# Kernel optimization log

Hardware: AMD Instinct MI355X
Metric: run time of the kernel (lower is better)

## Reference

```python
import jax, jax.numpy as jnp
import numpy as np

N_NODES = 100000
IN_F = 128
HID = [128, 128]
EMB = 64
N_EDGES = 3200000


def _glorot(key, fan_in, fan_out):
    lim = np.sqrt(6.0 / (fan_in + fan_out)).astype(np.float32)
    return jax.random.uniform(key, (fan_in, fan_out), jnp.float32, -lim, lim)


def setup_inputs() -> dict:
    key = jax.random.key(0)
    ks = jax.random.split(key, 10)
    h0 = jax.random.normal(ks[0], (N_NODES, IN_F), jnp.float32)
    edge_index = jax.random.randint(ks[1], (2, N_EDGES), 0, N_NODES, jnp.int32)
    edge_weight = jax.random.uniform(ks[2], (N_EDGES,), jnp.float32)
    dims = [(IN_F, HID[0]), (IN_F, HID[0]), (IN_F, HID[0]),
            (HID[0], HID[1]), (HID[0], HID[1]), (HID[1], EMB)]
    out = {"h0": h0, "edge_index": edge_index, "edge_weight": edge_weight}
    for i, (fi, fo) in enumerate(dims):
        out[f"W{i+1}"] = _glorot(ks[3 + i], fi, fo)
        out[f"b{i+1}"] = jnp.zeros((fo,), jnp.float32)
    return out


def gcn_conv(x, W, b, row, col, norm):
    # x: [N,F_in]; row/col/norm already include self-loops and symmetric norm
    h = x @ W                                  # [N, F_out]
    msg = h[row] * norm[:, None]               # gather + scale  [E+N, F_out]
    agg = jax.ops.segment_sum(msg, col, num_segments=x.shape[0])
    return agg + b


def reference(h0, edge_index, edge_weight, W1, b1, W2, b2, W3, b3, W4, b4, W5, b5, W6, b6):
    n = h0.shape[0]
    row, col = edge_index[0], edge_index[1]
    loop = jnp.arange(n, dtype=row.dtype)
    row2 = jnp.concatenate([row, loop])
    col2 = jnp.concatenate([col, loop])
    ew2 = jnp.concatenate([edge_weight, jnp.ones((n,), edge_weight.dtype)])
    # PyG gcn_norm: deg over destination, symmetric D^-1/2 A D^-1/2
    deg = jax.ops.segment_sum(ew2, col2, num_segments=n)
    dis = jnp.where(deg > 0, jax.lax.rsqrt(jnp.maximum(deg, 1e-20)), 0.0)
    norm = dis[row2] * ew2 * dis[col2]

    h1 = jnp.tanh(gcn_conv(h0, W1, b1, row2, col2, norm))
    h2 = jnp.tanh(gcn_conv(h0, W2, b2, row2, col2, norm))
    h3 = jnp.tanh(gcn_conv(h0, W3, b3, row2, col2, norm))
    h123 = h1 * h2 * h3
    h4 = jnp.tanh(gcn_conv(h123, W4, b4, row2, col2, norm))
    h5 = jnp.tanh(gcn_conv(h123, W5, b5, row2, col2, norm))
    h6 = jnp.tanh(gcn_conv(h4 * h5, W6, b6, row2, col2, norm))
    return h6
```

## Files before the change

### kernel.cpp

```cpp
#include <hip/hip_runtime.h>
#include <hip/hip_bf16.h>
#include <hip/hip_fp16.h>

constexpr int FDIM = 128;
#define HSCALE 16384.0f
#define HSCALE_INV (1.0f/16384.0f)
#define ZSCALE 0.125f
#define ZSCALE_COMP (HSCALE_INV * 8.0f)

typedef _Float16 f16x8 __attribute__((ext_vector_type(8)));
typedef float f32x4 __attribute__((ext_vector_type(4)));

constexpr int CHUNK = 4096;
constexpr int B1 = 64;
constexpr int B2 = 64;
constexpr int NC2 = 64;
constexpr int MAXC2 = 20;

__global__ __launch_bounds__(256) void k_p1hist(const int* __restrict__ col,
                                                int* __restrict__ cnt1, int E, int NB1)
{
    __shared__ int h[B1];
    int blk = blockIdx.x, t = threadIdx.x;
    if (t < B1) h[t] = 0;
    __syncthreads();
    int base = blk * CHUNK;
    for (int i = t; i < CHUNK; i += 256) {
        int g = base + i;
        if (g < E) atomicAdd(&h[col[g] >> 11], 1);
    }
    __syncthreads();
    if (t < B1) cnt1[t * NB1 + blk] = h[t];
}

__global__ __launch_bounds__(256) void k_blocksum(const int* __restrict__ cnt,
                                                  int* __restrict__ bsum, int n)
{
    __shared__ int s[256];
    int t = threadIdx.x;
    int i = blockIdx.x * 256 + t;
    s[t] = (i < n) ? cnt[i] : 0;
    __syncthreads();
    for (int o = 128; o > 0; o >>= 1) {
        if (t < o) s[t] += s[t + o];
        __syncthreads();
    }
    if (t == 0) bsum[blockIdx.x] = s[0];
}

__global__ __launch_bounds__(1024) void k_scan_bsum(const int* __restrict__ bsum,
                                                    int* __restrict__ boff, int nb,
                                                    int* __restrict__ out, int n, int total)
{
    __shared__ int s[1024];
    int t = threadIdx.x;
    int v = (t < nb) ? bsum[t] : 0;
    s[t] = v;
    __syncthreads();
    for (int o = 1; o < 1024; o <<= 1) {
        int u = (t >= o) ? s[t - o] : 0;
        __syncthreads();
        s[t] += u;
        __syncthreads();
    }
    if (t < nb) boff[t] = s[t] - v;
    if (t == 0) out[n] = total;
}

__global__ __launch_bounds__(256) void k_offsets(const int* __restrict__ cnt,
                                                 const int* __restrict__ boff,
                                                 int* __restrict__ out, int n)
{
    __shared__ int s[256];
    int t = threadIdx.x;
    int i = blockIdx.x * 256 + t;
    int v = (i < n) ? cnt[i] : 0;
    s[t] = v;
    __syncthreads();
    for (int o = 1; o < 256; o <<= 1) {
        int u = (t >= o) ? s[t - o] : 0;
        __syncthreads();
        s[t] += u;
        __syncthreads();
    }
    if (i < n) out[i] = boff[blockIdx.x] + s[t] - v;
}

__global__ __launch_bounds__(256) void k_p1part(const int* __restrict__ col,
                                                const int* __restrict__ row,
                                                const float* __restrict__ ew,
                                                const int* __restrict__ cnt1,
                                                const int* __restrict__ scan1,
                                                unsigned long long* __restrict__ rec1,
                                                int E, int NB1)
{
    __shared__ unsigned long long stage[CHUNK];
    __shared__ int hcnt[B1], lb[B1], gb[B1], cur[B1];
    int blk = blockIdx.x, t = threadIdx.x;
    if (t < B1) {
        hcnt[t] = cnt1[t * NB1 + blk];
        gb[t]   = scan1[t * NB1 + blk];
    }
    __syncthreads();
    if (t == 0) {
        int run = 0;
        for (int b = 0; b < B1; ++b) { lb[b] = run; run += hcnt[b]; }
    }
    __syncthreads();
    if (t < B1) cur[t] = lb[t];
    __syncthreads();
    int base = blk * CHUNK;
    for (int i = t; i < CHUNK; i += 256) {
        int g = base + i;
        if (g < E) {
            int c = col[g], r = row[g];
            unsigned long long rc = ((unsigned long long)c << 47) |
                                    ((unsigned long long)r << 30) |
                                    (unsigned long long)__half_as_ushort(__float2half(ew[g]));
            int p = atomicAdd(&cur[c >> 11], 1);
            stage[p] = rc;
        }
    }
    __syncthreads();
    int here = min(CHUNK, E - base);
    for (int j = t; j < here; j += 256) {
        unsigned long long rc = stage[j];
        int b = (int)(rc >> 58);
        rec1[gb[b] + (j - lb[b])] = rc;
    }
}

__global__ __launch_bounds__(256) void k_p2hist(const unsigned long long* __restrict__ rec1,
                                                const int* __restrict__ scan1,
                                                int* __restrict__ cnt2, int NB1)
{
    __shared__ int h[B2];
    int b = blockIdx.x / MAXC2, ci = blockIdx.x % MAXC2, t = threadIdx.x;
    int S1 = scan1[b * NB1];
    int S2 = scan1[(b + 1) * NB1];
    int size = S2 - S1;
    for (int c = ci; c * CHUNK < size && c < NC2; c += MAXC2) {
        __syncthreads();
        if (t < B2) h[t] = 0;
        __syncthreads();
        int cb = S1 + c * CHUNK, ce = min(cb + CHUNK, S2);
        for (int i = cb + t; i < ce; i += 256)
            atomicAdd(&h[(int)((rec1[i] >> 52) & 63)], 1);
        __syncthreads();
        if (t < B2) cnt2[(b * B2 + t) * NC2 + c] = h[t];
    }
}

__global__ __launch_bounds__(256) void k_p2part(const unsigned long long* __restrict__ rec1,
                                                const int* __restrict__ scan1,
                                                const int* __restrict__ cnt2,
                                                const int* __restrict__ scan2,
                                                unsigned long long* __restrict__ rec2, int NB1)
{
    __shared__ unsigned long long stage[CHUNK];
    __shared__ int hcnt[B2], lb[B2], gb[B2], cur[B2];
    int b = blockIdx.x / MAXC2, ci = blockIdx.x % MAXC2, t = threadIdx.x;
    int S1 = scan1[b * NB1];
    int S2 = scan1[(b + 1) * NB1];
    int size = S2 - S1;
    for (int c = ci; c * CHUNK < size && c < NC2; c += MAXC2) {
        __syncthreads();
        if (t < B2) {
            hcnt[t] = cnt2[(b * B2 + t) * NC2 + c];
            gb[t]   = scan2[(b * B2 + t) * NC2 + c];
        }
        __syncthreads();
        if (t == 0) {
            int run = 0;
            for (int sb = 0; sb < B2; ++sb) { lb[sb] = run; run += hcnt[sb]; }
        }
        __syncthreads();
        if (t < B2) cur[t] = lb[t];
        __syncthreads();
        int cb = S1 + c * CHUNK, ce = min(cb + CHUNK, S2);
        for (int i = cb + t; i < ce; i += 256) {
            unsigned long long rc = rec1[i];
            int p = atomicAdd(&cur[(int)((rc >> 52) & 63)], 1);
            stage[p] = rc;
        }
        __syncthreads();
        int here = ce - cb;
        for (int j = t; j < here; j += 256) {
            unsigned long long rc = stage[j];
            int sb = (int)((rc >> 52) & 63);
            rec2[gb[sb] + (j - lb[sb])] = rc;
        }
    }
}

__global__ __launch_bounds__(256) void k_p3(const unsigned long long* __restrict__ rec2,
                                            const int* __restrict__ scan2,
                                            int2* __restrict__ ep, int* __restrict__ off,
                                            float* __restrict__ dis, int N, int E)
{
    __shared__ int h[32], lb[32], cur[32];
    __shared__ float dg[32], sdis[32];
    int g = blockIdx.x, t = threadIdx.x;
    int S1 = scan2[g * NC2];
    int S2 = scan2[(g + 1) * NC2];
    if (t < 32) { h[t] = 0; dg[t] = 0.f; }
    __syncthreads();
    for (int i = S1 + t; i < S2; i += 256) {
        unsigned long long rc = rec2[i];
        int nl = (int)((rc >> 47) & 31);
        atomicAdd(&h[nl], 1);
        atomicAdd(&dg[nl], __half2float(__ushort_as_half((unsigned short)(rc & 0xFFFF))));
    }
    __syncthreads();
    if (t == 0) {
        int run = S1;
        for (int k = 0; k < 32; ++k) { lb[k] = run; run += h[k]; }
    }
    __syncthreads();
    if (t < 32) {
        cur[t] = lb[t];
        sdis[t] = 1.0f / sqrtf(dg[t] + 1.0f);
        int node = g * 32 + t;
        if (node < N) { off[node] = lb[t]; dis[node] = sdis[t]; }
    }
    if (g == 0 && t == 0) off[N] = E;
    __syncthreads();
    for (int i = S1 + t; i < S2; i += 256) {
        unsigned long long rc = rec2[i];
        int nl = (int)((rc >> 47) & 31);
        int p = atomicAdd(&cur[nl], 1);
        float w = __half2float(__ushort_as_half((unsigned short)(rc & 0xFFFF))) * sdis[nl];
        ep[p] = make_int2((int)((rc >> 30) & 0x1FFFF), __float_as_int(w));
    }
}

__global__ __launch_bounds__(256) void k_cvt(const float4* __restrict__ in,
                                             const float* __restrict__ dis,
                                             __half2* __restrict__ out, int n4)
{
    int i = blockIdx.x * 256 + threadIdx.x;
    if (i >= n4) return;
    float4 v = in[i];
    float d = dis[i >> 5];
    __half2 a = __floats2half2_rn(v.x * d, v.y * d);
    __half2 b = __floats2half2_rn(v.z * d, v.w * d);
    float2 pk;
    ((__half2*)&pk)[0] = a;
    ((__half2*)&pk)[1] = b;
    *(float2*)&out[(size_t)i * 2] = pk;
}

__global__ __launch_bounds__(256) void k_wt(const float* __restrict__ W,
                                            __half* __restrict__ Wt, int N)
{
    int idx = blockIdx.x * 256 + threadIdx.x;
    if (idx >= N * 128) return;
    int n = idx >> 7, k = idx & 127;
    Wt[idx] = __float2half(W[(size_t)k * N + n]);
}

__global__ __launch_bounds__(256) void k_spmm(const __half2* __restrict__ Xh,
                                              const int2* __restrict__ ep,
                                              const int* __restrict__ off,
                                              const float* __restrict__ dis,
                                              __half2* __restrict__ Yh, int n)
{
    int gt = blockIdx.x * 256 + threadIdx.x;
    int node = gt >> 6;
    int lane = threadIdx.x & 63;
    if (node >= n) return;

    float sn = dis[node];
    float2 x0 = __half22float2(Xh[(size_t)node * 64 + lane]);
    float a0x = sn * x0.x, a0y = sn * x0.y;
    float a1x = 0.f, a1y = 0.f;
    float a2x = 0.f, a2y = 0.f;
    float a3x = 0.f, a3y = 0.f;

    const int e0 = off[node];
    const int cnt = off[node + 1] - e0;
    const int2* el = ep + e0;
    const int nb = cnt >> 2;
    int done = 0;

    if (nb >= 2) {
        int2 q0, q1, q2, q3;
        int2 p0 = el[0], p1 = el[1], p2 = el[2], p3 = el[3];
        q0 = el[4]; q1 = el[5]; q2 = el[6]; q3 = el[7];
        __half2 xc0 = Xh[(size_t)p0.x * 64 + lane];
        __half2 xc1 = Xh[(size_t)p1.x * 64 + lane];
        __half2 xc2 = Xh[(size_t)p2.x * 64 + lane];
        __half2 xc3 = Xh[(size_t)p3.x * 64 + lane];
        float wc0 = __int_as_float(p0.y), wc1 = __int_as_float(p1.y);
        float wc2 = __int_as_float(p2.y), wc3 = __int_as_float(p3.y);

        int b;
        #pragma unroll 2
        for (b = 0; b + 2 < nb; ++b) {
            __half2 xn0 = Xh[(size_t)q0.x * 64 + lane];
            __half2 xn1 = Xh[(size_t)q1.x * 64 + lane];
            __half2 xn2 = Xh[(size_t)q2.x * 64 + lane];
            __half2 xn3 = Xh[(size_t)q3.x * 64 + lane];
            float wn0 = __int_as_float(q0.y), wn1 = __int_as_float(q1.y);
            float wn2 = __int_as_float(q2.y), wn3 = __int_as_float(q3.y);
            const int2* eb = el + (size_t)(b + 2) * 4;
            q0 = eb[0]; q1 = eb[1]; q2 = eb[2]; q3 = eb[3];
            float2 f0 = __half22float2(xc0), f1 = __half22float2(xc1);
            float2 f2 = __half22float2(xc2), f3 = __half22float2(xc3);
            a0x += wc0 * f0.x; a0y += wc0 * f0.y;
            a1x += wc1 * f1.x; a1y += wc1 * f1.y;
            a2x += wc2 * f2.x; a2y += wc2 * f2.y;
            a3x += wc3 * f3.x; a3y += wc3 * f3.y;
            xc0 = xn0; xc1 = xn1; xc2 = xn2; xc3 = xn3;
            wc0 = wn0; wc1 = wn1; wc2 = wn2; wc3 = wn3;
        }
        __half2 xn0 = Xh[(size_t)q0.x * 64 + lane];
        __half2 xn1 = Xh[(size_t)q1.x * 64 + lane];
        __half2 xn2 = Xh[(size_t)q2.x * 64 + lane];
        __half2 xn3 = Xh[(size_t)q3.x * 64 + lane];
        float wn0 = __int_as_float(q0.y), wn1 = __int_as_float(q1.y);
        float wn2 = __int_as_float(q2.y), wn3 = __int_as_float(q3.y);
        {
            float2 f0 = __half22float2(xc0), f1 = __half22float2(xc1);
            float2 f2 = __half22float2(xc2), f3 = __half22float2(xc3);
            a0x += wc0 * f0.x; a0y += wc0 * f0.y;
            a1x += wc1 * f1.x; a1y += wc1 * f1.y;
            a2x += wc2 * f2.x; a2y += wc2 * f2.y;
            a3x += wc3 * f3.x; a3y += wc3 * f3.y;
        }
        {
            float2 f0 = __half22float2(xn0), f1 = __half22float2(xn1);
            float2 f2 = __half22float2(xn2), f3 = __half22float2(xn3);
            a0x += wn0 * f0.x; a0y += wn0 * f0.y;
            a1x += wn1 * f1.x; a1y += wn1 * f1.y;
            a2x += wn2 * f2.x; a2y += wn2 * f2.y;
            a3x += wn3 * f3.x; a3y += wn3 * f3.y;
        }
        done = nb * 4;
    }
    for (int e = done; e < cnt; ++e) {
        int2 p = el[e];
        float2 xv = __half22float2(Xh[(size_t)p.x * 64 + lane]);
        float w = __int_as_float(p.y);
        a0x += w * xv.x; a0y += w * xv.y;
    }
    float rx = (a0x + a1x) + (a2x + a3x);
    float ry = (a0y + a1y) + (a2y + a3y);
    Yh[(size_t)node * 64 + lane] = __floats2half2_rn(rx, ry);
}

__global__ __launch_bounds__(256) void k_spmm64(const __half* __restrict__ Zh,
                                                const int2* __restrict__ ep,
                                                const int* __restrict__ off,
                                                const float* __restrict__ dis,
                                                const float* __restrict__ b6,
                                                float* __restrict__ out, int n)
{
    int gt = blockIdx.x * 256 + threadIdx.x;
    int node = gt >> 6;
    int lane = threadIdx.x & 63;
    if (node >= n) return;

    float sn = dis[node];
    float x0 = __half2float(Zh[(size_t)node * 64 + lane]);
    float a0 = sn * x0, a1 = 0.f, a2 = 0.f, a3 = 0.f;

    const int e0 = off[node];
    const int cnt = off[node + 1] - e0;
    const int2* el = ep + e0;
    const int nb = cnt >> 2;
    int done = 0;

    if (nb >= 2) {
        int2 q0, q1, q2, q3;
        int2 p0 = el[0], p1 = el[1], p2 = el[2], p3 = el[3];
        q0 = el[4]; q1 = el[5]; q2 = el[6]; q3 = el[7];
        __half xc0 = Zh[(size_t)p0.x * 64 + lane];
        __half xc1 = Zh[(size_t)p1.x * 64 + lane];
        __half xc2 = Zh[(size_t)p2.x * 64 + lane];
        __half xc3 = Zh[(size_t)p3.x * 64 + lane];
        float wc0 = __int_as_float(p0.y), wc1 = __int_as_float(p1.y);
        float wc2 = __int_as_float(p2.y), wc3 = __int_as_float(p3.y);

        int b;
        #pragma unroll 2
        for (b = 0; b + 2 < nb; ++b) {
            __half xn0 = Zh[(size_t)q0.x * 64 + lane];
            __half xn1 = Zh[(size_t)q1.x * 64 + lane];
            __half xn2 = Zh[(size_t)q2.x * 64 + lane];
            __half xn3 = Zh[(size_t)q3.x * 64 + lane];
            float wn0 = __int_as_float(q0.y), wn1 = __int_as_float(q1.y);
            float wn2 = __int_as_float(q2.y), wn3 = __int_as_float(q3.y);
            const int2* eb = el + (size_t)(b + 2) * 4;
            q0 = eb[0]; q1 = eb[1]; q2 = eb[2]; q3 = eb[3];
            a0 += wc0 * __half2float(xc0);
            a1 += wc1 * __half2float(xc1);
            a2 += wc2 * __half2float(xc2);
            a3 += wc3 * __half2float(xc3);
            xc0 = xn0; xc1 = xn1; xc2 = xn2; xc3 = xn3;
            wc0 = wn0; wc1 = wn1; wc2 = wn2; wc3 = wn3;
        }
        __half xn0 = Zh[(size_t)q0.x * 64 + lane];
        __half xn1 = Zh[(size_t)q1.x * 64 + lane];
        __half xn2 = Zh[(size_t)q2.x * 64 + lane];
        __half xn3 = Zh[(size_t)q3.x * 64 + lane];
        float wn0 = __int_as_float(q0.y), wn1 = __int_as_float(q1.y);
        float wn2 = __int_as_float(q2.y), wn3 = __int_as_float(q3.y);
        a0 += wc0 * __half2float(xc0);
        a1 += wc1 * __half2float(xc1);
        a2 += wc2 * __half2float(xc2);
        a3 += wc3 * __half2float(xc3);
        a0 += wn0 * __half2float(xn0);
        a1 += wn1 * __half2float(xn1);
        a2 += wn2 * __half2float(xn2);
        a3 += wn3 * __half2float(xn3);
        done = nb * 4;
    }
    for (int e = done; e < cnt; ++e) {
        int2 p = el[e];
        float w = __int_as_float(p.y);
        a0 += w * __half2float(Zh[(size_t)p.x * 64 + lane]);
    }
    float acc = (a0 + a1) + (a2 + a3);
    out[(size_t)node * 64 + lane] = tanhf(fmaf(acc, ZSCALE_COMP, b6[lane]));
}

__device__ __forceinline__ float fast_tanh(float x) {
    float e = __expf(2.0f * x);
    return 1.0f - 2.0f * __builtin_amdgcn_rcpf(e + 1.0f);
}

template <int FOUT, int NW, bool ACT>
__global__ __launch_bounds__(256, 2) void k_mgemm(const __half* __restrict__ Yh,
                                                  float IS, float OS,
                                                  const float* __restrict__ dis,
                                                  const __half* __restrict__ Wt0, const float* __restrict__ B0,
                                                  const __half* __restrict__ Wt1, const float* __restrict__ B1,
                                                  const __half* __restrict__ Wt2, const float* __restrict__ B2,
                                                  __half* __restrict__ Out, int nRows)
{
    constexpr int NF = FOUT / 16;
    constexpr int FPW = NF / 4;
    int tid = threadIdx.x;
    int wv = tid >> 6;
    int lane = tid & 63;
    int lo = lane & 15, hi = lane >> 4;
    int r0 = blockIdx.x * 64;

    const __half* Wts[3] = {Wt0, Wt1, Wt2};
    const float*  Bs[3]  = {B0, B1, B2};

    f16x8 bfr[FPW][NW][4];
    float bias[FPW][NW];
    #pragma unroll
    for (int fp = 0; fp < FPW; ++fp) {
        int f = wv * FPW + fp;
        #pragma unroll
        for (int w = 0; w < NW; ++w) {
            const __half* Bp = Wts[w] + (size_t)(f * 16 + lo) * 128 + hi * 8;
            #pragma unroll
            for (int ks = 0; ks < 4; ++ks)
                bfr[fp][w][ks] = *(const f16x8*)(Bp + ks * 32);
            if constexpr (ACT) bias[fp][w] = Bs[w][f * 16 + lo];
        }
    }

    float disr[4][4];
    if constexpr (ACT) {
        #pragma unroll
        for (int rt = 0; rt < 4; ++rt)
            #pragma unroll
            for (int r = 0; r < 4; ++r) {
                int row = r0 + rt * 16 + hi * 4 + r;
                if (row >= nRows) row = nRows - 1;
                disr[rt][r] = dis[row];
            }
    }

    f16x8 a[4], an[4];
    {
        int row = r0 + lo;
        if (row >= nRows) row = nRows - 1;
        const __half* Ap = Yh + (size_t)row * 128 + hi * 8;
        #pragma unroll
        for (int ks = 0; ks < 4; ++ks) a[ks] = *(const f16x8*)(Ap + ks * 32);
    }

    #pragma unroll
    for (int rt = 0; rt < 4; ++rt) {
        if (rt < 3) {
            int row = r0 + (rt + 1) * 16 + lo;
            if (row >= nRows) row = nRows - 1;
            const __half* Ap = Yh + (size_t)row * 128 + hi * 8;
            #pragma unroll
            for (int ks = 0; ks < 4; ++ks) an[ks] = *(const f16x8*)(Ap + ks * 32);
        }
        #pragma unroll
        for (int fp = 0; fp < FPW; ++fp) {
            f32x4 ac0 = {0.f, 0.f, 0.f, 0.f};
            f32x4 ac1 = {0.f, 0.f, 0.f, 0.f};
            f32x4 ac2 = {0.f, 0.f, 0.f, 0.f};
            #pragma unroll
            for (int ks = 0; ks < 4; ++ks) {
                ac0 = __builtin_amdgcn_mfma_f32_16x16x32_f16(a[ks], bfr[fp][0][ks], ac0, 0, 0, 0);
                if constexpr (NW > 1)
                    ac1 = __builtin_amdgcn_mfma_f32_16x16x32_f16(a[ks], bfr[fp][1][ks], ac1, 0, 0, 0);
                if constexpr (NW > 2)
                    ac2 = __builtin_amdgcn_mfma_f32_16x16x32_f16(a[ks], bfr[fp][2][ks], ac2, 0, 0, 0);
            }
            int c = (wv * FPW + fp) * 16 + lo;
            #pragma unroll
            for (int r = 0; r < 4; ++r) {
                int row = r0 + rt * 16 + hi * 4 + r;
                float v;
                if constexpr (ACT) {
                    v = fast_tanh(fmaf(ac0[r], IS, bias[fp][0]));
                    if constexpr (NW > 1) v *= fast_tanh(fmaf(ac1[r], IS, bias[fp][1]));
                    if constexpr (NW > 2) v *= fast_tanh(fmaf(ac2[r], IS, bias[fp][2]));
                    v *= OS * disr[rt][r];
                } else {
                    v = ac0[r] * OS;
                }
                if (row < nRows)
                    Out[(size_t)row * FOUT + c] = __float2half(v);
            }
        }
        #pragma unroll
        for (int ks = 0; ks < 4; ++ks) a[ks] = an[ks];
    }
}

extern "C" void kernel_launch(void* const* d_in, const int* in_sizes, int n_in,
                              void* d_out, int out_size, void* d_ws, size_t ws_size,
                              hipStream_t stream)
{
    const float* h0 = (const float*)d_in[0];
    const int*   ei = (const int*)d_in[1];
    const float* ew = (const float*)d_in[2];
    const float* W1 = (const float*)d_in[3];  const float* b1 = (const float*)d_in[4];
    const float* W2 = (const float*)d_in[5];  const float* b2 = (const float*)d_in[6];
    const float* W3 = (const float*)d_in[7];  const float* b3 = (const float*)d_in[8];
    const float* W4 = (const float*)d_in[9];  const float* b4 = (const float*)d_in[10];
    const float* W5 = (const float*)d_in[11]; const float* b5 = (const float*)d_in[12];
    const float* W6 = (const float*)d_in[13]; const float* b6 = (const float*)d_in[14];

    const int N = in_sizes[0] / FDIM;
    const int E = in_sizes[2];
    const int* rowp = ei;
    const int* colp = ei + E;

    const int NB1 = (E + CHUNK - 1) / CHUNK;
    const int n1  = B1 * NB1;
    const int n2  = B1 * B2 * NC2;
    const int NBs1 = (n1 + 255) / 256;
    const int NBs2 = (n2 + 255) / 256;

    char* p = (char*)d_ws;
    auto alloc = [&](size_t bytes) -> void* {
        void* r = (void*)p;
        p += (bytes + 255) & ~(size_t)255;
        return r;
    };
    int* cnt1  = (int*)alloc((size_t)(n1 + 1) * 4);
    int* scan1 = (int*)alloc((size_t)(n1 + 1) * 4);
    int* cnt2  = (int*)alloc((size_t)(n2 + 1) * 4);
    int* scan2 = (int*)alloc((size_t)(n2 + 1) * 4);
    int* bsum  = (int*)alloc((size_t)1024 * 4);
    int* boff  = (int*)alloc((size_t)1024 * 4);
    int* off   = (int*)alloc((size_t)(N + 1) * 4);
    float* dis = (float*)alloc((size_t)N * 4);
    unsigned long long* rec1 = (unsigned long long*)alloc((size_t)E * 8);
    unsigned long long* rec2 = (unsigned long long*)alloc((size_t)E * 8);
    __half2* Xh = (__half2*)alloc((size_t)N * FDIM * 2);
    __half2* Hh = (__half2*)alloc((size_t)N * FDIM * 2);
    __half* W1t = (__half*)alloc((size_t)128 * 128 * 2);
    __half* W2t = (__half*)alloc((size_t)128 * 128 * 2);
    __half* W3t = (__half*)alloc((size_t)128 * 128 * 2);
    __half* W4t = (__half*)alloc((size_t)128 * 128 * 2);
    __half* W5t = (__half*)alloc((size_t)128 * 128 * 2);
    __half* W6t = (__half*)alloc((size_t)64 * 128 * 2);

    int2*    ep = (int2*)rec1;
    __half2* Yh = (__half2*)rec2;
    __half*  Zh = (__half*)Xh;

    hipMemsetAsync(cnt2, 0, (size_t)(n2 + 1) * 4, stream);

    k_p1hist<<<NB1, 256, 0, stream>>>(colp, cnt1, E, NB1);
    k_blocksum<<<NBs1, 256, 0, stream>>>(cnt1, bsum, n1);
    k_scan_bsum<<<1, 1024, 0, stream>>>(bsum, boff, NBs1, scan1, n1, E);
    k_offsets<<<NBs1, 256, 0, stream>>>(cnt1, boff, scan1, n1);
    k_p1part<<<NB1, 256, 0, stream>>>(colp, rowp, ew, cnt1, scan1, rec1, E, NB1);
    k_p2hist<<<B1 * MAXC2, 256, 0, stream>>>(rec1, scan1, cnt2, NB1);
    k_blocksum<<<NBs2, 256, 0, stream>>>(cnt2, bsum, n2);
    k_scan_bsum<<<1, 1024, 0, stream>>>(bsum, boff, NBs2, scan2, n2, E);
    k_offsets<<<NBs2, 256, 0, stream>>>(cnt2, boff, scan2, n2);
    k_p2part<<<B1 * MAXC2, 256, 0, stream>>>(rec1, scan1, cnt2, scan2, rec2, NB1);
    k_p3<<<B1 * B2, 256, 0, stream>>>(rec2, scan2, ep, off, dis, N, E);

    k_cvt<<<(N * 32 + 255) / 256, 256, 0, stream>>>((const float4*)h0, dis, Xh, N * 32);
    k_wt<<<64, 256, 0, stream>>>(W1, W1t, 128);
    k_wt<<<64, 256, 0, stream>>>(W2, W2t, 128);
    k_wt<<<64, 256, 0, stream>>>(W3, W3t, 128);
    k_wt<<<64, 256, 0, stream>>>(W4, W4t, 128);
    k_wt<<<64, 256, 0, stream>>>(W5, W5t, 128);
    k_wt<<<32, 256, 0, stream>>>(W6, W6t, 64);

    const int sb = (N + 3) / 4;
    const int gb = (N + 63) / 64;

    k_spmm<<<sb, 256, 0, stream>>>(Xh, ep, off, dis, Yh, N);
    k_mgemm<128, 3, true><<<gb, 256, 0, stream>>>((const __half*)Yh, 1.0f, HSCALE, dis,
        W1t, b1, W2t, b2, W3t, b3, (__half*)Hh, N);
    k_spmm<<<sb, 256, 0, stream>>>(Hh, ep, off, dis, Yh, N);
    k_mgemm<128, 2, true><<<gb, 256, 0, stream>>>((const __half*)Yh, HSCALE_INV, HSCALE, dis,
        W4t, b4, W5t, b5, nullptr, nullptr, (__half*)Hh, N);
    k_mgemm<64, 1, false><<<gb, 256, 0, stream>>>((const __half*)Hh, 1.0f, ZSCALE, nullptr,
        W6t, b6, nullptr, nullptr, nullptr, nullptr, Zh, N);
    k_spmm64<<<sb, 256, 0, stream>>>(Zh, ep, off, dis, b6, (float*)d_out, N);
}
```

Measured before the change: 518.7 us.

## Split each wavefront into two half-waves processing alternating edges with wider loads

Both SpMM kernels now assign each half of a 64-lane wavefront to alternate edges of a node. Each lane loads 8 bytes (4 halves) in the 128-wide kernel, or 4 bytes in the 64-wide one, instead of 4 or 2 bytes. The two halves' partial sums are combined with a cross-half shuffle before the store. The goal is to double the number of independent gathers in flight per wave and use wider vector loads and packed FMAs, which should hide gather latency better. In exchange the code adds shuffle and reduction overhead, a clamped tail loop that wastes lanes on odd edge counts, and extra padding on the edge buffer.

After: 522.6 us. About the same (+0.7%).

```diff
diff --git a/kernel.cpp b/kernel.cpp
--- a/kernel.cpp
+++ b/kernel.cpp
@@ -10,6 +10,7 @@
 
 typedef _Float16 f16x8 __attribute__((ext_vector_type(8)));
 typedef float f32x4 __attribute__((ext_vector_type(4)));
+typedef float f32x2 __attribute__((ext_vector_type(2)));
 
 constexpr int CHUNK = 4096;
 constexpr int B1 = 64;
@@ -269,84 +270,108 @@
     int node = gt >> 6;
     int lane = threadIdx.x & 63;
     if (node >= n) return;
-
-    float sn = dis[node];
-    float2 x0 = __half22float2(Xh[(size_t)node * 64 + lane]);
-    float a0x = sn * x0.x, a0y = sn * x0.y;
-    float a1x = 0.f, a1y = 0.f;
-    float a2x = 0.f, a2y = 0.f;
-    float a3x = 0.f, a3y = 0.f;
+    const int half = lane >> 5;
+    const int l31 = lane & 31;
+    const char* Xb = (const char*)Xh;
+    const unsigned loff = (unsigned)l31 << 3;
+
+    f32x2 p0a = {0.f, 0.f}, p0b = {0.f, 0.f};
+    f32x2 p1a = {0.f, 0.f}, p1b = {0.f, 0.f};
+
+    if (half == 0) {
+        float sn = dis[node];
+        float2 raw = *(const float2*)(Xb + ((unsigned)node << 8) + loff);
+        float2 f0 = __half22float2(((const __half2*)&raw)[0]);
+        float2 f1 = __half22float2(((const __half2*)&raw)[1]);
+        p0a.x = sn * f0.x; p0a.y = sn * f0.y;
+        p0b.x = sn * f1.x; p0b.y = sn * f1.y;
+    }
 
     const int e0 = off[node];
     const int cnt = off[node + 1] - e0;
     const int2* el = ep + e0;
-    const int nb = cnt >> 2;
+    const int nb = cnt >> 3;
     int done = 0;
 
+#define SPMM_FMA(XV, WV)                                                     \
+    {                                                                        \
+        _Pragma("unroll")                                                    \
+        for (int j = 0; j < 4; ++j) {                                        \
+            float2 f0 = __half22float2(((const __half2*)&XV[j])[0]);         \
+            float2 f1 = __half22float2(((const __half2*)&XV[j])[1]);         \
+            f32x2 wv = {WV[j], WV[j]};                                       \
+            f32x2 v0 = {f0.x, f0.y}, v1 = {f1.x, f1.y};                      \
+            if (j & 1) { p1a += wv * v0; p1b += wv * v1; }                   \
+            else       { p0a += wv * v0; p0b += wv * v1; }                   \
+        }                                                                    \
+    }
+
     if (nb >= 2) {
-        int2 q0, q1, q2, q3;
-        int2 p0 = el[0], p1 = el[1], p2 = el[2], p3 = el[3];
-        q0 = el[4]; q1 = el[5]; q2 = el[6]; q3 = el[7];
-        __half2 xc0 = Xh[(size_t)p0.x * 64 + lane];
-        __half2 xc1 = Xh[(size_t)p1.x * 64 + lane];
-        __half2 xc2 = Xh[(size_t)p2.x * 64 + lane];
-        __half2 xc3 = Xh[(size_t)p3.x * 64 + lane];
-        float wc0 = __int_as_float(p0.y), wc1 = __int_as_float(p1.y);
-        float wc2 = __int_as_float(p2.y), wc3 = __int_as_float(p3.y);
-
-        int b;
+        int2 en[4];
+        float2 xc[4], g[4];
+        float wc[4], w2[4];
+        {
+            int2 ec[4];
+            #pragma unroll
+            for (int j = 0; j < 4; ++j) ec[j] = el[2 * j + half];
+            #pragma unroll
+            for (int j = 0; j < 4; ++j)
+                xc[j] = *(const float2*)(Xb + ((unsigned)ec[j].x << 8) + loff);
+            #pragma unroll
+            for (int j = 0; j < 4; ++j) wc[j] = __int_as_float(ec[j].y);
+        }
+        #pragma unroll
+        for (int j = 0; j < 4; ++j) en[j] = el[8 + 2 * j + half];
+
         #pragma unroll 2
-        for (b = 0; b + 2 < nb; ++b) {
-            __half2 xn0 = Xh[(size_t)q0.x * 64 + lane];
-            __half2 xn1 = Xh[(size_t)q1.x * 64 + lane];
-            __half2 xn2 = Xh[(size_t)q2.x * 64 + lane];
-            __half2 xn3 = Xh[(size_t)q3.x * 64 + lane];
-            float wn0 = __int_as_float(q0.y), wn1 = __int_as_float(q1.y);
-            float wn2 = __int_as_float(q2.y), wn3 = __int_as_float(q3.y);
-            const int2* eb = el + (size_t)(b + 2) * 4;
-            q0 = eb[0]; q1 = eb[1]; q2 = eb[2]; q3 = eb[3];
-            float2 f0 = __half22float2(xc0), f1 = __half22float2(xc1);
-            float2 f2 = __half22float2(xc2), f3 = __half22float2(xc3);
-            a0x += wc0 * f0.x; a0y += wc0 * f0.y;
-            a1x += wc1 * f1.x; a1y += wc1 * f1.y;
-            a2x += wc2 * f2.x; a2y += wc2 * f2.y;
-            a3x += wc3 * f3.x; a3y += wc3 * f3.y;
-            xc0 = xn0; xc1 = xn1; xc2 = xn2; xc3 = xn3;
-            wc0 = wn0; wc1 = wn1; wc2 = wn2; wc3 = wn3;
-        }
-        __half2 xn0 = Xh[(size_t)q0.x * 64 + lane];
-        __half2 xn1 = Xh[(size_t)q1.x * 64 + lane];
-        __half2 xn2 = Xh[(size_t)q2.x * 64 + lane];
-        __half2 xn3 = Xh[(size_t)q3.x * 64 + lane];
-        float wn0 = __int_as_float(q0.y), wn1 = __int_as_float(q1.y);
-        float wn2 = __int_as_float(q2.y), wn3 = __int_as_float(q3.y);
-        {
-            float2 f0 = __half22float2(xc0), f1 = __half22float2(xc1);
-            float2 f2 = __half22float2(xc2), f3 = __half22float2(xc3);
-            a0x += wc0 * f0.x; a0y += wc0 * f0.y;
-            a1x += wc1 * f1.x; a1y += wc1 * f1.y;
-            a2x += wc2 * f2.x; a2y += wc2 * f2.y;
-            a3x += wc3 * f3.x; a3y += wc3 * f3.y;
-        }
-        {
-            float2 f0 = __half22float2(xn0), f1 = __half22float2(xn1);
-            float2 f2 = __half22float2(xn2), f3 = __half22float2(xn3);
-            a0x += wn0 * f0.x; a0y += wn0 * f0.y;
-            a1x += wn1 * f1.x; a1y += wn1 * f1.y;
-            a2x += wn2 * f2.x; a2y += wn2 * f2.y;
-            a3x += wn3 * f3.x; a3y += wn3 * f3.y;
-        }
-        done = nb * 4;
-    }
-    for (int e = done; e < cnt; ++e) {
-        int2 p = el[e];
-        float2 xv = __half22float2(Xh[(size_t)p.x * 64 + lane]);
-        float w = __int_as_float(p.y);
-        a0x += w * xv.x; a0y += w * xv.y;
-    }
-    float rx = (a0x + a1x) + (a2x + a3x);
-    float ry = (a0y + a1y) + (a2y + a3y);
-    Yh[(size_t)node * 64 + lane] = __floats2half2_rn(rx, ry);
+        for (int b = 0; b + 2 < nb; ++b) {
+            #pragma unroll
+            for (int j = 0; j < 4; ++j)
+                g[j] = *(const float2*)(Xb + ((unsigned)en[j].x << 8) + loff);
+            #pragma unroll
+            for (int j = 0; j < 4; ++j) w2[j] = __int_as_float(en[j].y);
+            const int2* eb = el + (b + 2) * 8;
+            #pragma unroll
+            for (int j = 0; j < 4; ++j) en[j] = eb[2 * j + half];
+            SPMM_FMA(xc, wc);
+            #pragma unroll
+            for (int j = 0; j < 4; ++j) { xc[j] = g[j]; wc[j] = w2[j]; }
+        }
+        #pragma unroll
+        for (int j = 0; j < 4; ++j)
+            g[j] = *(const float2*)(Xb + ((unsigned)en[j].x << 8) + loff);
+        #pragma unroll
+        for (int j = 0; j < 4; ++j) w2[j] = __int_as_float(en[j].y);
+        SPMM_FMA(xc, wc);
+        SPMM_FMA(g, w2);
+        done = nb * 8;
+    }
+    for (int e = done; e < cnt; e += 2) {
+        int idx = e + half;
+        int idc = min(idx, cnt - 1);
+        int2 pe = el[idc];
+        float w = (idx < cnt) ? __int_as_float(pe.y) : 0.f;
+        float2 raw = *(const float2*)(Xb + ((unsigned)pe.x << 8) + loff);
+        float2 f0 = __half22float2(((const __half2*)&raw)[0]);
+        float2 f1 = __half22float2(((const __half2*)&raw)[1]);
+        f32x2 wv = {w, w};
+        f32x2 v0 = {f0.x, f0.y}, v1 = {f1.x, f1.y};
+        p0a += wv * v0; p0b += wv * v1;
+    }
+#undef SPMM_FMA
+
+    float r0 = p0a.x + p1a.x, r1 = p0a.y + p1a.y;
+    float r2 = p0b.x + p1b.x, r3 = p0b.y + p1b.y;
+    r0 += __shfl_xor(r0, 32);
+    r1 += __shfl_xor(r1, 32);
+    r2 += __shfl_xor(r2, 32);
+    r3 += __shfl_xor(r3, 32);
+    if (half == 0) {
+        float2 pk;
+        ((__half2*)&pk)[0] = __floats2half2_rn(r0, r1);
+        ((__half2*)&pk)[1] = __floats2half2_rn(r2, r3);
+        *(float2*)((char*)Yh + ((unsigned)node << 8) + loff) = pk;
+    }
 }
 
 __global__ __launch_bounds__(256) void k_spmm64(const __half* __restrict__ Zh,
@@ -360,69 +385,100 @@
     int node = gt >> 6;
     int lane = threadIdx.x & 63;
     if (node >= n) return;
-
-    float sn = dis[node];
-    float x0 = __half2float(Zh[(size_t)node * 64 + lane]);
-    float a0 = sn * x0, a1 = 0.f, a2 = 0.f, a3 = 0.f;
+    const int half = lane >> 5;
+    const int l31 = lane & 31;
+    const char* Zb = (const char*)Zh;
+    const unsigned loff = (unsigned)l31 << 2;
+
+    f32x2 p0 = {0.f, 0.f}, p1 = {0.f, 0.f};
+
+    if (half == 0) {
+        float sn = dis[node];
+        __half2 raw = *(const __half2*)(Zb + ((unsigned)node << 7) + loff);
+        float2 f0 = __half22float2(raw);
+        p0.x = sn * f0.x; p0.y = sn * f0.y;
+    }
 
     const int e0 = off[node];
     const int cnt = off[node + 1] - e0;
     const int2* el = ep + e0;
-    const int nb = cnt >> 2;
+    const int nb = cnt >> 3;
     int done = 0;
 
+#define SPMM64_FMA(XV, WV)                                                   \
+    {                                                                        \
+        _Pragma("unroll")                                                    \
+        for (int j = 0; j < 4; ++j) {                                        \
+            float2 f0 = __half22float2(XV[j]);                               \
+            f32x2 wv = {WV[j], WV[j]};                                       \
+            f32x2 v0 = {f0.x, f0.y};                                         \
+            if (j & 1) p1 += wv * v0; else p0 += wv * v0;                    \
+        }                                                                    \
+    }
+
     if (nb >= 2) {
-        int2 q0, q1, q2, q3;
-        int2 p0 = el[0], p1 = el[1], p2 = el[2], p3 = el[3];
-        q0 = el[4]; q1 = el[5]; q2 = el[6]; q3 = el[7];
-        __half xc0 = Zh[(size_t)p0.x * 64 + lane];
-        __half xc1 = Zh[(size_t)p1.x * 64 + lane];
-        __half xc2 = Zh[(size_t)p2.x * 64 + lane];
-        __half xc3 = Zh[(size_t)p3.x * 64 + lane];
-        float wc0 = __int_as_float(p0.y), wc1 = __int_as_float(p1.y);
-        float wc2 = __int_as_float(p2.y), wc3 = __int_as_float(p3.y);
-
-        int b;
+        int2 en[4];
+        __half2 xc[4], g[4];
+        float wc[4], w2[4];
+        {
+            int2 ec[4];
+            #pragma unroll
+            for (int j = 0; j < 4; ++j) ec[j] = el[2 * j + half];
+            #pragma unroll
+            for (int j = 0; j < 4; ++j)
+                xc[j] = *(const __half2*)(Zb + ((unsigned)ec[j].x << 7) + loff);
+            #pragma unroll
+            for (int j = 0; j < 4; ++j) wc[j] = __int_as_float(ec[j].y);
+        }
+        #pragma unroll
+        for (int j = 0; j < 4; ++j) en[j] = el[8 + 2 * j + half];
+
         #pragma unroll 2
-        for (b = 0; b + 2 < nb; ++b) {
-            __half xn0 = Zh[(size_t)q0.x * 64 + lane];
-            __half xn1 = Zh[(size_t)q1.x * 64 + lane];
-            __half xn2 = Zh[(size_t)q2.x * 64 + lane];
-            __half xn3 = Zh[(size_t)q3.x * 64 + lane];
-            float wn0 = __int_as_float(q0.y), wn1 = __int_as_float(q1.y);
-            float wn2 = __int_as_float(q2.y), wn3 = __int_as_float(q3.y);
-            const int2* eb = el + (size_t)(b + 2) * 4;
-            q0 = eb[0]; q1 = eb[1]; q2 = eb[2]; q3 = eb[3];
-            a0 += wc0 * __half2float(xc0);
-            a1 += wc1 * __half2float(xc1);
-            a2 += wc2 * __half2float(xc2);
-            a3 += wc3 * __half2float(xc3);
-            xc0 = xn0; xc1 = xn1; xc2 = xn2; xc3 = xn3;
-            wc0 = wn0; wc1 = wn1; wc2 = wn2; wc3 = wn3;
-        }
-        __half xn0 = Zh[(size_t)q0.x * 64 + lane];
-        __half xn1 = Zh[(size_t)q1.x * 64 + lane];
-        __half xn2 = Zh[(size_t)q2.x * 64 + lane];
-        __half xn3 = Zh[(size_t)q3.x * 64 + lane];
-        float wn0 = __int_as_float(q0.y), wn1 = __int_as_float(q1.y);
-        float wn2 = __int_as_float(q2.y), wn3 = __int_as_float(q3.y);
-        a0 += wc0 * __half2float(xc0);
-        a1 += wc1 * __half2float(xc1);
-        a2 += wc2 * __half2float(xc2);
-        a3 += wc3 * __half2float(xc3);
-        a0 += wn0 * __half2float(xn0);
-        a1 += wn1 * __half2float(xn1);
-        a2 += wn2 * __half2float(xn2);
-        a3 += wn3 * __half2float(xn3);
-        done = nb * 4;
-    }
-    for (int e = done; e < cnt; ++e) {
-        int2 p = el[e];
-        float w = __int_as_float(p.y);
-        a0 += w * __half2float(Zh[(size_t)p.x * 64 + lane]);
-    }
-    float acc = (a0 + a1) + (a2 + a3);
-    out[(size_t)node * 64 + lane] = tanhf(fmaf(acc, ZSCALE_COMP, b6[lane]));
+        for (int b = 0; b + 2 < nb; ++b) {
+            #pragma unroll
+            for (int j = 0; j < 4; ++j)
+                g[j] = *(const __half2*)(Zb + ((unsigned)en[j].x << 7) + loff);
+            #pragma unroll
+            for (int j = 0; j < 4; ++j) w2[j] = __int_as_float(en[j].y);
+            const int2* eb = el + (b + 2) * 8;
+            #pragma unroll
+            for (int j = 0; j < 4; ++j) en[j] = eb[2 * j + half];
+            SPMM64_FMA(xc, wc);
+            #pragma unroll
+            for (int j = 0; j < 4; ++j) { xc[j] = g[j]; wc[j] = w2[j]; }
+        }
+        #pragma unroll
+        for (int j = 0; j < 4; ++j)
+            g[j] = *(const __half2*)(Zb + ((unsigned)en[j].x << 7) + loff);
+        #pragma unroll
+        for (int j = 0; j < 4; ++j) w2[j] = __int_as_float(en[j].y);
+        SPMM64_FMA(xc, wc);
+        SPMM64_FMA(g, w2);
+        done = nb * 8;
+    }
+    for (int e = done; e < cnt; e += 2) {
+        int idx = e + half;
+        int idc = min(idx, cnt - 1);
+        int2 pe = el[idc];
+        float w = (idx < cnt) ? __int_as_float(pe.y) : 0.f;
+        __half2 raw = *(const __half2*)(Zb + ((unsigned)pe.x << 7) + loff);
+        float2 f0 = __half22float2(raw);
+        f32x2 wv = {w, w};
+        f32x2 v0 = {f0.x, f0.y};
+        p0 += wv * v0;
+    }
+#undef SPMM64_FMA
+
+    float r0 = p0.x + p1.x, r1 = p0.y + p1.y;
+    r0 += __shfl_xor(r0, 32);
+    r1 += __shfl_xor(r1, 32);
+    if (half == 0) {
+        float2 bb = *(const float2*)(b6 + 2 * l31);
+        float2 o;
+        o.x = tanhf(fmaf(r0, ZSCALE_COMP, bb.x));
+        o.y = tanhf(fmaf(r1, ZSCALE_COMP, bb.y));
+        *(float2*)((char*)out + ((unsigned)node << 8) + ((unsigned)l31 << 3)) = o;
+    }
 }
 
 __device__ __forceinline__ float fast_tanh(float x) {
@@ -569,7 +625,7 @@
     int* boff  = (int*)alloc((size_t)1024 * 4);
     int* off   = (int*)alloc((size_t)(N + 1) * 4);
     float* dis = (float*)alloc((size_t)N * 4);
-    unsigned long long* rec1 = (unsigned long long*)alloc((size_t)E * 8);
+    unsigned long long* rec1 = (unsigned long long*)alloc((size_t)(E + 16) * 8);
     unsigned long long* rec2 = (unsigned long long*)alloc((size_t)E * 8);
     __half2* Xh = (__half2*)alloc((size_t)N * FDIM * 2);
     __half2* Hh = (__half2*)alloc((size_t)N * FDIM * 2);
```
